# Kernel tuning notes

Measured on AMD Instinct MI355X. Metric: run time of the kernel, lower is better.

The kernel has to match this reference:

```python
import jax, jax.numpy as jnp
import numpy as np

N, IC, IH, IW = 8, 128, 32, 32
OC, H, KH, KW = 32, 256, 2, 2


def setup_inputs() -> dict:
    key = jax.random.key(0)
    ks = jax.random.split(key, 7)
    s1 = 1.0 / np.sqrt(IC)
    s2 = 1.0 / np.sqrt(H)
    x = jax.random.normal(ks[0], (N, IC, IH, IW), dtype=jnp.float32)
    # per-output-channel MLP params, stacked along oC (torch Linear-style uniform init)
    W1 = jax.random.uniform(ks[1], (OC, IC, H), jnp.float32, -s1, s1)
    b1 = jax.random.uniform(ks[2], (OC, H), jnp.float32, -s1, s1)
    W2 = jax.random.uniform(ks[3], (OC, H, H), jnp.float32, -s2, s2)
    b2 = jax.random.uniform(ks[4], (OC, H), jnp.float32, -s2, s2)
    W3 = jax.random.uniform(ks[5], (OC, H, KH * KW), jnp.float32, -s2, s2)
    b3 = jax.random.uniform(ks[6], (OC, KH * KW), jnp.float32, -s2, s2)
    return {"x": x, "W1": W1, "b1": b1, "W2": W2, "b2": b2, "W3": W3, "b3": b3}


def reference(x, W1, b1, W2, b2, W3, b3):
    n, iC, iH, iW = x.shape
    oC = W1.shape[0]
    kH, kW = KH, KW
    # per-pixel features: [n, iH, iW, iC]
    pix = jnp.transpose(x, (0, 2, 3, 1))
    # batched 3-layer MLP over stacked oC channels (single grouped GEMM per layer)
    h1 = jax.nn.relu(jnp.einsum('nijc,ocd->onijd', pix, W1) + b1[:, None, None, None, :])
    h2 = jax.nn.relu(jnp.einsum('onijd,ode->onije', h1, W2) + b2[:, None, None, None, :])
    out = jnp.einsum('onije,oek->onijk', h2, W3) + b3[:, None, None, None, :]
    # [oC, n, iH, iW, kH, kW] -> [n, oC, iH, kH, iW, kW] -> [n, oC, oH, oW]
    out = out.reshape(oC, n, iH, iW, kH, kW)
    out = jnp.transpose(out, (1, 0, 2, 4, 3, 5)).reshape(n, oC, kH * iH, kW * iW)
    return out
```

## Files before the change

### kernel.cpp

```cpp
#include <hip/hip_runtime.h>
#include <hip/hip_bf16.h>


#define IC    128
#define IHW   1024
#define OCH   32
#define HDIM  256

typedef float  f32x4  __attribute__((ext_vector_type(4)));
typedef float  f32x2  __attribute__((ext_vector_type(2)));
typedef __bf16 bf16x8 __attribute__((ext_vector_type(8)));
typedef unsigned short us8 __attribute__((ext_vector_type(8)));
typedef unsigned int u32;

static __device__ __forceinline__ unsigned short f2bf(float f) {
  __hip_bfloat16 h = __float2bfloat16(f);
  return __builtin_bit_cast(unsigned short, h);
}

static __device__ __forceinline__ u32 cvtpk(float lo, float hi) {
  u32 r;
  asm("v_cvt_pk_bf16_f32 %0, %1, %2" : "=v"(r) : "v"(lo), "v"(hi));
  return r;
}

static __device__ __forceinline__ bf16x8 ld16(const unsigned short* p) {
  return __builtin_bit_cast(bf16x8, *reinterpret_cast<const uint4*>(p));
}

static __device__ __forceinline__ void gl_lds16(const unsigned short* g, char* l) {
  __builtin_amdgcn_global_load_lds(
      (const __attribute__((address_space(1))) u32*)g,
      (__attribute__((address_space(3))) u32*)l,
      16, 0, 0);
}

__global__ __launch_bounds__(256) void transpose_bf16_k(
    const float* __restrict__ src, unsigned short* __restrict__ dst,
    int NR, int NC, int nrt, int nct)
{
  __shared__ float tl[64 * 65];
  const int bid = blockIdx.x;
  const int ct = bid % nct;
  const int rt = (bid / nct) % nrt;
  const int b  = bid / (nct * nrt);
  const int t  = threadIdx.x;

  const float* sb = src + ((size_t)b * NR + (rt << 6)) * NC + (ct << 6);
  const int col = (t & 15) << 2;
  const int rq  = t >> 4;
#pragma unroll
  for (int rr = 0; rr < 4; ++rr) {
    int row = (rr << 4) + rq;
    f32x4 v = *reinterpret_cast<const f32x4*>(sb + row * NC + col);
#pragma unroll
    for (int i = 0; i < 4; ++i) tl[row * 65 + col + i] = v[i];
  }
  __syncthreads();

  unsigned short* db = dst + ((size_t)b * NC + (ct << 6)) * NR + (rt << 6);
  const int r0 = (t & 7) << 3;
  const int cq = t >> 3;
#pragma unroll
  for (int cr = 0; cr < 2; ++cr) {
    int c = (cr << 5) + cq;
    us8 vv;
#pragma unroll
    for (int i = 0; i < 8; ++i) vv[i] = f2bf(tl[(r0 + i) * 65 + c]);
    *reinterpret_cast<us8*>(db + (size_t)c * NR + r0) = vv;
  }
}

__global__ void conv_w3_k(const float* __restrict__ W3, unsigned short* __restrict__ W3t) {
  int idx = blockIdx.x * 256 + threadIdx.x;
  int k = idx & 255;
  int nn = (idx >> 8) & 15;
  int o = idx >> 12;
  W3t[idx] = (nn < 4) ? f2bf(W3[(o * HDIM + k) * 4 + nn]) : (unsigned short)0;
}


#define LDB(dst, buf, ROW, ks)                                                   \
  _Pragma("unroll")                                                              \
  for (int mf = 0; mf < 2; ++mf) {                                               \
    int m = (mf << 4) + l15;                                                     \
    dst[mf] = *reinterpret_cast<const bf16x8*>(                                  \
        (buf) + ((((m << (ROW)) + ((ks) << 6) + (kgrp << 1))) ^ ((l15 & 7) << 4)));\
  }

#define MF4(WR, KS, BP)                                                          \
  __builtin_amdgcn_s_setprio(1);                                                 \
  _Pragma("unroll")                                                              \
  for (int nf = 0; nf < 2; ++nf)                                                 \
    _Pragma("unroll")                                                            \
    for (int mf = 0; mf < 2; ++mf)                                               \
      acc[nf][mf] = __builtin_amdgcn_mfma_f32_16x16x32_bf16(WR[nf][KS], BP[mf], acc[nf][mf], 0, 0, 0); \
  __builtin_amdgcn_s_setprio(0);

#define EPI(dst)                                                                 \
  _Pragma("unroll")                                                              \
  for (int nf = 0; nf < 2; ++nf) {                                               \
    int n0 = wnb + (nf << 4) + (lg << 2);                                        \
    _Pragma("unroll")                                                            \
    for (int mf = 0; mf < 2; ++mf) {                                             \
      int m = (mf << 4) + l15;                                                   \
      uint2 hv;                                                                  \
      hv.x = cvtpk(fmaxf(acc[nf][mf][0], 0.f), fmaxf(acc[nf][mf][1], 0.f));      \
      hv.y = cvtpk(fmaxf(acc[nf][mf][2], 0.f), fmaxf(acc[nf][mf][3], 0.f));      \
      *reinterpret_cast<uint2*>(                                                 \
          (dst) + (((m << 9) + (n0 << 1)) ^ ((l15 & 7) << 4))) = hv;             \
    }                                                                            \
  }

#define INIT_ACC(BB)                                                             \
  _Pragma("unroll")                                                              \
  for (int nf = 0; nf < 2; ++nf)                                                 \
    _Pragma("unroll")                                                            \
    for (int mf = 0; mf < 2; ++mf) acc[nf][mf] = BB[nf];

#define STAGE(PXB, BUF)                                                          \
  {                                                                              \
    int m = t >> 4, c16 = t & 15;                                                \
    gl_lds16(pix + (size_t)((PXB) + m) * IC + ((c16 ^ (m & 7)) << 3),            \
             (BUF) + t * 16);                                                    \
  }

__global__ __launch_bounds__(512, 2) void fused_mlp_k(
    const unsigned short* __restrict__ pix,
    const unsigned short* __restrict__ W1t,
    const unsigned short* __restrict__ W2t,
    const unsigned short* __restrict__ W3t,
    const float* __restrict__ b1,
    const float* __restrict__ b2,
    const float* __restrict__ b3f,
    float* __restrict__ out)
{
  __shared__ __align__(16) char lds[81920];
  const int t    = threadIdx.x;
  const int lane = t & 63;
  const int w    = t >> 6;
  const int bx   = blockIdx.x;
  const int o    = ((bx & 7) << 2) | ((bx >> 3) & 3);
  const int pixbase = (bx >> 5) << 8;

  const int l15  = lane & 15;
  const int lg   = lane >> 4;
  const int kgrp = lg << 3;
  const int wnb  = w << 5;

  char* pixb[2] = { lds,         lds + 8192 };
  char* h1b[2]  = { lds + 16384, lds + 32768 };
  char* h2b[2]  = { lds + 49152, lds + 65536 };

  STAGE(pixbase,      pixb[0])
  STAGE(pixbase + 32, pixb[1])

  const unsigned short* W1p = W1t + (o << 15) + (wnb + l15) * IC + kgrp;
  const unsigned short* W2p = W2t + (o << 16) + (wnb + l15) * HDIM + kgrp;
  bf16x8 W1r[2][4], W2r[2][8];
#pragma unroll
  for (int nf = 0; nf < 2; ++nf)
#pragma unroll
    for (int ks = 0; ks < 4; ++ks)
      W1r[nf][ks] = ld16(W1p + (nf << 4) * IC + (ks << 5));
#pragma unroll
  for (int nf = 0; nf < 2; ++nf)
#pragma unroll
    for (int ks = 0; ks < 8; ++ks)
      W2r[nf][ks] = ld16(W2p + (nf << 4) * HDIM + (ks << 5));

  f32x4 bb1[2], bb2[2];
#pragma unroll
  for (int nf = 0; nf < 2; ++nf) {
    bb1[nf] = *reinterpret_cast<const f32x4*>(b1 + (o << 8) + wnb + (nf << 4) + (lg << 2));
    bb2[nf] = *reinterpret_cast<const f32x4*>(b2 + (o << 8) + wnb + (nf << 4) + (lg << 2));
  }
  const f32x4 b3v = *reinterpret_cast<const f32x4*>(b3f + (o << 2));

  f32x4 acc[2][2];
  bf16x8 bp[2], bq[2];

  __syncthreads();

  INIT_ACC(bb1)
  LDB(bp, pixb[0], 8, 0)
  LDB(bq, pixb[0], 8, 1) MF4(W1r, 0, bp)
  LDB(bp, pixb[0], 8, 2) MF4(W1r, 1, bq)
  LDB(bq, pixb[0], 8, 3) MF4(W1r, 2, bp)
                         MF4(W1r, 3, bq)
  EPI(h1b[0])
  __syncthreads();

#pragma unroll
  for (int i = 0; i <= 8; ++i) {
    if (i <= 5) STAGE(pixbase + ((i + 2) << 5), pixb[i & 1])

    if (i <= 7) {
      char* src = h1b[i & 1];
      INIT_ACC(bb2)
      LDB(bp, src, 9, 0)
      LDB(bq, src, 9, 1) MF4(W2r, 0, bp)
      LDB(bp, src, 9, 2) MF4(W2r, 1, bq)
      LDB(bq, src, 9, 3) MF4(W2r, 2, bp)
      LDB(bp, src, 9, 4) MF4(W2r, 3, bq)
      LDB(bq, src, 9, 5) MF4(W2r, 4, bp)
      LDB(bp, src, 9, 6) MF4(W2r, 5, bq)
      LDB(bq, src, 9, 7) MF4(W2r, 6, bp)
                         MF4(W2r, 7, bq)
      EPI(h2b[i & 1])
    }

    if (i >= 1 && w < 2) {
      const char* hs = h2b[(i - 1) & 1];
      const unsigned short* W3p = W3t + (o << 12) + l15 * HDIM + kgrp;
      const int m3 = (w << 4) + l15;
      f32x4 a3a = b3v;
      f32x4 a3b = {0.f, 0.f, 0.f, 0.f};
      bf16x8 w3f0 = ld16(W3p), w3f1 = ld16(W3p + 32);
      bf16x8 bh0 = *reinterpret_cast<const bf16x8*>(
          hs + (((m3 << 9) + (kgrp << 1)) ^ ((l15 & 7) << 4)));
      bf16x8 bh1 = *reinterpret_cast<const bf16x8*>(
          hs + (((m3 << 9) + (1 << 6) + (kgrp << 1)) ^ ((l15 & 7) << 4)));
#pragma unroll
      for (int ks = 0; ks < 8; ks += 2) {
        bf16x8 wnA, bnA, wnB, bnB;
        if (ks < 6) {
          wnA = ld16(W3p + ((ks + 2) << 5));
          bnA = *reinterpret_cast<const bf16x8*>(
              hs + (((m3 << 9) + ((ks + 2) << 6) + (kgrp << 1)) ^ ((l15 & 7) << 4)));
          wnB = ld16(W3p + ((ks + 3) << 5));
          bnB = *reinterpret_cast<const bf16x8*>(
              hs + (((m3 << 9) + ((ks + 3) << 6) + (kgrp << 1)) ^ ((l15 & 7) << 4)));
        }
        a3a = __builtin_amdgcn_mfma_f32_16x16x32_bf16(w3f0, bh0, a3a, 0, 0, 0);
        a3b = __builtin_amdgcn_mfma_f32_16x16x32_bf16(w3f1, bh1, a3b, 0, 0, 0);
        w3f0 = wnA; bh0 = bnA; w3f1 = wnB; bh1 = bnB;
      }
      if (lane < 16) {
        int pixel = pixbase + ((i - 1) << 5) + m3;
        int n = pixel >> 10, p = pixel & 1023;
        int ii = p >> 5, jj = p & 31;
        float* ob = out + ((size_t)((n << 5) + o) << 12) + (ii << 7) + (jj << 1);
        f32x2 r0 = { a3a[0] + a3b[0], a3a[1] + a3b[1] };
        f32x2 r1 = { a3a[2] + a3b[2], a3a[3] + a3b[3] };
        *reinterpret_cast<f32x2*>(ob) = r0;
        *reinterpret_cast<f32x2*>(ob + 64) = r1;
      }
    }

    if (i <= 6) {
      char* psrc = pixb[(i + 1) & 1];
      INIT_ACC(bb1)
      LDB(bp, psrc, 8, 0)
      LDB(bq, psrc, 8, 1) MF4(W1r, 0, bp)
      LDB(bp, psrc, 8, 2) MF4(W1r, 1, bq)
      LDB(bq, psrc, 8, 3) MF4(W1r, 2, bp)
                          MF4(W1r, 3, bq)
      EPI(h1b[(i + 1) & 1])
    }

    __syncthreads();
  }
}

extern "C" void kernel_launch(void* const* d_in, const int* in_sizes, int n_in,
                              void* d_out, int out_size, void* d_ws, size_t ws_size,
                              hipStream_t stream) {
  const float* x  = (const float*)d_in[0];
  const float* W1 = (const float*)d_in[1];
  const float* b1 = (const float*)d_in[2];
  const float* W2 = (const float*)d_in[3];
  const float* b2 = (const float*)d_in[4];
  const float* W3 = (const float*)d_in[5];
  const float* b3 = (const float*)d_in[6];
  float* out = (float*)d_out;

  char* ws = (char*)d_ws;
  unsigned short* pixw = (unsigned short*)(ws);
  unsigned short* W1t  = (unsigned short*)(ws + (size_t)(2u << 20));
  unsigned short* W2t  = (unsigned short*)(ws + (size_t)(4u << 20));
  unsigned short* W3t  = (unsigned short*)(ws + (size_t)(8u << 20));

  transpose_bf16_k<<<8 * 2 * 16, 256, 0, stream>>>(x, pixw, 128, 1024, 2, 16);
  transpose_bf16_k<<<32 * 2 * 4, 256, 0, stream>>>(W1, W1t, 128, 256, 2, 4);
  transpose_bf16_k<<<32 * 4 * 4, 256, 0, stream>>>(W2, W2t, 256, 256, 4, 4);
  conv_w3_k<<<512, 256, 0, stream>>>(W3, W3t);

  fused_mlp_k<<<1024, 512, 0, stream>>>(pixw, W1t, W2t, W3t, b1, b2, b3, out);
}
```

Measured before the change: 92.79 us.

## Fuse layer-3 into layer-2 epilogue via register shuffles and partial sums

Instead of writing h2 to LDS and having two waves run the full K=256 layer-3 GEMM, each wave now converts its h2 accumulator slice to bf16 in registers. It rearranges that slice with cross-lane shuffles into an MFMA B-fragment and runs a single 16x16x32 MFMA against its slice of W3, which is held in a register. The per-wave partial outputs go to a small LDS buffer, and one wave sums the eight partials and adds the bias before storing. This removes the h2 LDS round trip, cuts LDS use from 80KB to 56KB, and spreads layer-3 work across all waves, at the cost of shuffle overhead and a serialized reduction done by a single wave.

```diff
diff --git a/kernel.cpp b/kernel.cpp
--- a/kernel.cpp
+++ b/kernel.cpp
@@ -135,7 +135,7 @@
     const float* __restrict__ b3f,
     float* __restrict__ out)
 {
-  __shared__ __align__(16) char lds[81920];
+  __shared__ __align__(16) char lds[57344];
   const int t    = threadIdx.x;
   const int lane = t & 63;
   const int w    = t >> 6;
@@ -150,7 +150,7 @@
 
   char* pixb[2] = { lds,         lds + 8192 };
   char* h1b[2]  = { lds + 16384, lds + 32768 };
-  char* h2b[2]  = { lds + 49152, lds + 65536 };
+  char* partb[2]= { lds + 49152, lds + 53248 };
 
   STAGE(pixbase,      pixb[0])
   STAGE(pixbase + 32, pixb[1])
@@ -169,6 +169,8 @@
     for (int ks = 0; ks < 8; ++ks)
       W2r[nf][ks] = ld16(W2p + (nf << 4) * HDIM + (ks << 5));
 
+  bf16x8 W3A = ld16(W3t + (o << 12) + l15 * HDIM + (w << 5) + kgrp);
+
   f32x4 bb1[2], bb2[2];
 #pragma unroll
   for (int nf = 0; nf < 2; ++nf) {
@@ -176,9 +178,14 @@
     bb2[nf] = *reinterpret_cast<const f32x4*>(b2 + (o << 8) + wnb + (nf << 4) + (lg << 2));
   }
   const f32x4 b3v = *reinterpret_cast<const f32x4*>(b3f + (o << 2));
+  const f32x4 vzero = {0.f, 0.f, 0.f, 0.f};
 
   f32x4 acc[2][2];
   bf16x8 bp[2], bq[2];
+
+  const int srcLo = (((lg << 1) & 3) << 4) + l15;
+  const int srcHi = ((((lg << 1) + 1) & 3) << 4) + l15;
+  const int sel   = lg >> 1;
 
   __syncthreads();
 
@@ -207,45 +214,46 @@
       LDB(bp, src, 9, 6) MF4(W2r, 5, bq)
       LDB(bq, src, 9, 7) MF4(W2r, 6, bp)
                          MF4(W2r, 7, bq)
-      EPI(h2b[i & 1])
+
+      char* pw = partb[i & 1];
+#pragma unroll
+      for (int mf = 0; mf < 2; ++mf) {
+        u32 p00 = cvtpk(fmaxf(acc[0][mf][0], 0.f), fmaxf(acc[0][mf][1], 0.f));
+        u32 p01 = cvtpk(fmaxf(acc[0][mf][2], 0.f), fmaxf(acc[0][mf][3], 0.f));
+        u32 p10 = cvtpk(fmaxf(acc[1][mf][0], 0.f), fmaxf(acc[1][mf][1], 0.f));
+        u32 p11 = cvtpk(fmaxf(acc[1][mf][2], 0.f), fmaxf(acc[1][mf][3], 0.f));
+        u32 a0 = __shfl((int)p00, srcLo, 64), c0 = __shfl((int)p10, srcLo, 64);
+        u32 a1 = __shfl((int)p01, srcLo, 64), c1 = __shfl((int)p11, srcLo, 64);
+        u32 a2 = __shfl((int)p00, srcHi, 64), c2 = __shfl((int)p10, srcHi, 64);
+        u32 a3 = __shfl((int)p01, srcHi, 64), c3 = __shfl((int)p11, srcHi, 64);
+        uint4 fr;
+        fr.x = sel ? c0 : a0;
+        fr.y = sel ? c1 : a1;
+        fr.z = sel ? c2 : a2;
+        fr.w = sel ? c3 : a3;
+        bf16x8 h2f = __builtin_bit_cast(bf16x8, fr);
+        f32x4 p3 = __builtin_amdgcn_mfma_f32_16x16x32_bf16(W3A, h2f, vzero, 0, 0, 0);
+        if (lane < 16)
+          *reinterpret_cast<f32x4*>(pw + (w << 9) + (mf << 8) + (l15 << 4)) = p3;
+      }
     }
 
-    if (i >= 1 && w < 2) {
-      const char* hs = h2b[(i - 1) & 1];
-      const unsigned short* W3p = W3t + (o << 12) + l15 * HDIM + kgrp;
-      const int m3 = (w << 4) + l15;
-      f32x4 a3a = b3v;
-      f32x4 a3b = {0.f, 0.f, 0.f, 0.f};
-      bf16x8 w3f0 = ld16(W3p), w3f1 = ld16(W3p + 32);
-      bf16x8 bh0 = *reinterpret_cast<const bf16x8*>(
-          hs + (((m3 << 9) + (kgrp << 1)) ^ ((l15 & 7) << 4)));
-      bf16x8 bh1 = *reinterpret_cast<const bf16x8*>(
-          hs + (((m3 << 9) + (1 << 6) + (kgrp << 1)) ^ ((l15 & 7) << 4)));
-#pragma unroll
-      for (int ks = 0; ks < 8; ks += 2) {
-        bf16x8 wnA, bnA, wnB, bnB;
-        if (ks < 6) {
-          wnA = ld16(W3p + ((ks + 2) << 5));
-          bnA = *reinterpret_cast<const bf16x8*>(
-              hs + (((m3 << 9) + ((ks + 2) << 6) + (kgrp << 1)) ^ ((l15 & 7) << 4)));
-          wnB = ld16(W3p + ((ks + 3) << 5));
-          bnB = *reinterpret_cast<const bf16x8*>(
-              hs + (((m3 << 9) + ((ks + 3) << 6) + (kgrp << 1)) ^ ((l15 & 7) << 4)));
-        }
-        a3a = __builtin_amdgcn_mfma_f32_16x16x32_bf16(w3f0, bh0, a3a, 0, 0, 0);
-        a3b = __builtin_amdgcn_mfma_f32_16x16x32_bf16(w3f1, bh1, a3b, 0, 0, 0);
-        w3f0 = wnA; bh0 = bnA; w3f1 = wnB; bh1 = bnB;
-      }
-      if (lane < 16) {
-        int pixel = pixbase + ((i - 1) << 5) + m3;
-        int n = pixel >> 10, p = pixel & 1023;
-        int ii = p >> 5, jj = p & 31;
-        float* ob = out + ((size_t)((n << 5) + o) << 12) + (ii << 7) + (jj << 1);
-        f32x2 r0 = { a3a[0] + a3b[0], a3a[1] + a3b[1] };
-        f32x2 r1 = { a3a[2] + a3b[2], a3a[3] + a3b[3] };
-        *reinterpret_cast<f32x2*>(ob) = r0;
-        *reinterpret_cast<f32x2*>(ob + 64) = r1;
-      }
+    if (i >= 1 && w == 7 && lane < 32) {
+      const char* pp = partb[(i - 1) & 1];
+      int px  = lane;
+      int mfp = px >> 4, l15p = px & 15;
+      f32x4 s = b3v;
+#pragma unroll
+      for (int ww = 0; ww < 8; ++ww)
+        s += *reinterpret_cast<const f32x4*>(pp + (ww << 9) + (mfp << 8) + (l15p << 4));
+      int pixel = pixbase + ((i - 1) << 5) + px;
+      int n = pixel >> 10, p = pixel & 1023;
+      int ii = p >> 5, jj = p & 31;
+      float* ob = out + ((size_t)((n << 5) + o) << 12) + (ii << 7) + (jj << 1);
+      f32x2 r0 = { s[0], s[1] };
+      f32x2 r1 = { s[2], s[3] };
+      *reinterpret_cast<f32x2*>(ob) = r0;
+      *reinterpret_cast<f32x2*>(ob + 64) = r1;
     }
 
     if (i <= 6) {
```

New measurement: 99.23 us. +6.9%, slower.

## Merge prepass kernels, triple-buffer pixel staging with vmcnt barriers, preload W3

Applied to the files above, without the earlier changes.

The four preprocessing launches (x, W1, W2 transposes and W3 conversion) become one prepass kernel that branches on block index, which cuts launch overhead. The fused MLP kernel now triple-buffers the pixel tiles in LDS and issues each prefetch later in the iteration. Its __syncthreads is replaced by a barrier that waits only on outstanding global loads up to a count, so one prefetch can stay in flight across the barrier. W3 fragments are loaded into registers once instead of on every iteration, which raises register pressure and LDS use (90 KB) at two blocks per CU.

```diff
diff --git a/kernel.cpp b/kernel.cpp
--- a/kernel.cpp
+++ b/kernel.cpp
@@ -35,48 +35,60 @@
       16, 0, 0);
 }
 
-__global__ __launch_bounds__(256) void transpose_bf16_k(
-    const float* __restrict__ src, unsigned short* __restrict__ dst,
-    int NR, int NC, int nrt, int nct)
+static __device__ void transpose_dev(const float* __restrict__ src,
+                                     unsigned short* __restrict__ dst,
+                                     int NR, int NC, int nrt, int nct,
+                                     int bid, int t, float* tl)
+{
+  const int ct = bid % nct;
+  const int rt = (bid / nct) % nrt;
+  const int b  = bid / (nct * nrt);
+
+  const float* sb = src + ((size_t)b * NR + (rt << 6)) * NC + (ct << 6);
+  const int col = (t & 15) << 2;
+  const int rq  = t >> 4;
+#pragma unroll
+  for (int rr = 0; rr < 4; ++rr) {
+    int row = (rr << 4) + rq;
+    f32x4 v = *reinterpret_cast<const f32x4*>(sb + row * NC + col);
+#pragma unroll
+    for (int i = 0; i < 4; ++i) tl[row * 65 + col + i] = v[i];
+  }
+  __syncthreads();
+
+  unsigned short* db = dst + ((size_t)b * NC + (ct << 6)) * NR + (rt << 6);
+  const int r0 = (t & 7) << 3;
+  const int cq = t >> 3;
+#pragma unroll
+  for (int cr = 0; cr < 2; ++cr) {
+    int c = (cr << 5) + cq;
+    us8 vv;
+#pragma unroll
+    for (int i = 0; i < 8; ++i) vv[i] = f2bf(tl[(r0 + i) * 65 + c]);
+    *reinterpret_cast<us8*>(db + (size_t)c * NR + r0) = vv;
+  }
+}
+
+__global__ __launch_bounds__(256) void prepass_k(
+    const float* __restrict__ x,  unsigned short* __restrict__ pix,
+    const float* __restrict__ W1, unsigned short* __restrict__ W1t,
+    const float* __restrict__ W2, unsigned short* __restrict__ W2t,
+    const float* __restrict__ W3, unsigned short* __restrict__ W3t)
 {
   __shared__ float tl[64 * 65];
   const int bid = blockIdx.x;
-  const int ct = bid % nct;
-  const int rt = (bid / nct) % nrt;
-  const int b  = bid / (nct * nrt);
-  const int t  = threadIdx.x;
-
-  const float* sb = src + ((size_t)b * NR + (rt << 6)) * NC + (ct << 6);
-  const int col = (t & 15) << 2;
-  const int rq  = t >> 4;
-#pragma unroll
-  for (int rr = 0; rr < 4; ++rr) {
-    int row = (rr << 4) + rq;
-    f32x4 v = *reinterpret_cast<const f32x4*>(sb + row * NC + col);
-#pragma unroll
-    for (int i = 0; i < 4; ++i) tl[row * 65 + col + i] = v[i];
-  }
-  __syncthreads();
-
-  unsigned short* db = dst + ((size_t)b * NC + (ct << 6)) * NR + (rt << 6);
-  const int r0 = (t & 7) << 3;
-  const int cq = t >> 3;
-#pragma unroll
-  for (int cr = 0; cr < 2; ++cr) {
-    int c = (cr << 5) + cq;
-    us8 vv;
-#pragma unroll
-    for (int i = 0; i < 8; ++i) vv[i] = f2bf(tl[(r0 + i) * 65 + c]);
-    *reinterpret_cast<us8*>(db + (size_t)c * NR + r0) = vv;
-  }
-}
-
-__global__ void conv_w3_k(const float* __restrict__ W3, unsigned short* __restrict__ W3t) {
-  int idx = blockIdx.x * 256 + threadIdx.x;
-  int k = idx & 255;
-  int nn = (idx >> 8) & 15;
-  int o = idx >> 12;
-  W3t[idx] = (nn < 4) ? f2bf(W3[(o * HDIM + k) * 4 + nn]) : (unsigned short)0;
+  const int t   = threadIdx.x;
+  if (bid < 256) {
+    transpose_dev(x, pix, 128, 1024, 2, 16, bid, t, tl);
+  } else if (bid < 512) {
+    transpose_dev(W1, W1t, 128, 256, 2, 4, bid - 256, t, tl);
+  } else if (bid < 1024) {
+    transpose_dev(W2, W2t, 256, 256, 4, 4, bid - 512, t, tl);
+  } else {
+    int idx = ((bid - 1024) << 8) + t;
+    int k = idx & 255, nn = (idx >> 8) & 15, o = idx >> 12;
+    W3t[idx] = (nn < 4) ? f2bf(W3[(o * HDIM + k) * 4 + nn]) : (unsigned short)0;
+  }
 }
 
 
@@ -125,6 +137,12 @@
              (BUF) + t * 16);                                                    \
   }
 
+#define PIPE_BARRIER(N)                                                          \
+  asm volatile("s_waitcnt vmcnt(" #N ") lgkmcnt(0)" ::: "memory");               \
+  __builtin_amdgcn_sched_barrier(0);                                             \
+  __builtin_amdgcn_s_barrier();                                                  \
+  __builtin_amdgcn_sched_barrier(0);
+
 __global__ __launch_bounds__(512, 2) void fused_mlp_k(
     const unsigned short* __restrict__ pix,
     const unsigned short* __restrict__ W1t,
@@ -135,7 +153,7 @@
     const float* __restrict__ b3f,
     float* __restrict__ out)
 {
-  __shared__ __align__(16) char lds[81920];
+  __shared__ __align__(16) char lds[90112];
   const int t    = threadIdx.x;
   const int lane = t & 63;
   const int w    = t >> 6;
@@ -148,16 +166,17 @@
   const int kgrp = lg << 3;
   const int wnb  = w << 5;
 
-  char* pixb[2] = { lds,         lds + 8192 };
-  char* h1b[2]  = { lds + 16384, lds + 32768 };
-  char* h2b[2]  = { lds + 49152, lds + 65536 };
+  char* pixb[3] = { lds, lds + 8192, lds + 16384 };
+  char* h1b[2]  = { lds + 24576, lds + 40960 };
+  char* h2b[2]  = { lds + 57344, lds + 73728 };
 
   STAGE(pixbase,      pixb[0])
   STAGE(pixbase + 32, pixb[1])
+  STAGE(pixbase + 64, pixb[2])
 
   const unsigned short* W1p = W1t + (o << 15) + (wnb + l15) * IC + kgrp;
   const unsigned short* W2p = W2t + (o << 16) + (wnb + l15) * HDIM + kgrp;
-  bf16x8 W1r[2][4], W2r[2][8];
+  bf16x8 W1r[2][4], W2r[2][8], W3r[8];
 #pragma unroll
   for (int nf = 0; nf < 2; ++nf)
 #pragma unroll
@@ -168,6 +187,9 @@
 #pragma unroll
     for (int ks = 0; ks < 8; ++ks)
       W2r[nf][ks] = ld16(W2p + (nf << 4) * HDIM + (ks << 5));
+#pragma unroll
+  for (int ks = 0; ks < 8; ++ks)
+    W3r[ks] = ld16(W3t + (o << 12) + l15 * HDIM + (ks << 5) + kgrp);
 
   f32x4 bb1[2], bb2[2];
 #pragma unroll
@@ -176,6 +198,7 @@
     bb2[nf] = *reinterpret_cast<const f32x4*>(b2 + (o << 8) + wnb + (nf << 4) + (lg << 2));
   }
   const f32x4 b3v = *reinterpret_cast<const f32x4*>(b3f + (o << 2));
+  const f32x4 vzero = {0.f, 0.f, 0.f, 0.f};
 
   f32x4 acc[2][2];
   bf16x8 bp[2], bq[2];
@@ -193,8 +216,6 @@
 
 #pragma unroll
   for (int i = 0; i <= 8; ++i) {
-    if (i <= 5) STAGE(pixbase + ((i + 2) << 5), pixb[i & 1])
-
     if (i <= 7) {
       char* src = h1b[i & 1];
       INIT_ACC(bb2)
@@ -212,29 +233,17 @@
 
     if (i >= 1 && w < 2) {
       const char* hs = h2b[(i - 1) & 1];
-      const unsigned short* W3p = W3t + (o << 12) + l15 * HDIM + kgrp;
       const int m3 = (w << 4) + l15;
       f32x4 a3a = b3v;
       f32x4 a3b = {0.f, 0.f, 0.f, 0.f};
-      bf16x8 w3f0 = ld16(W3p), w3f1 = ld16(W3p + 32);
-      bf16x8 bh0 = *reinterpret_cast<const bf16x8*>(
-          hs + (((m3 << 9) + (kgrp << 1)) ^ ((l15 & 7) << 4)));
-      bf16x8 bh1 = *reinterpret_cast<const bf16x8*>(
-          hs + (((m3 << 9) + (1 << 6) + (kgrp << 1)) ^ ((l15 & 7) << 4)));
 #pragma unroll
       for (int ks = 0; ks < 8; ks += 2) {
-        bf16x8 wnA, bnA, wnB, bnB;
-        if (ks < 6) {
-          wnA = ld16(W3p + ((ks + 2) << 5));
-          bnA = *reinterpret_cast<const bf16x8*>(
-              hs + (((m3 << 9) + ((ks + 2) << 6) + (kgrp << 1)) ^ ((l15 & 7) << 4)));
-          wnB = ld16(W3p + ((ks + 3) << 5));
-          bnB = *reinterpret_cast<const bf16x8*>(
-              hs + (((m3 << 9) + ((ks + 3) << 6) + (kgrp << 1)) ^ ((l15 & 7) << 4)));
-        }
-        a3a = __builtin_amdgcn_mfma_f32_16x16x32_bf16(w3f0, bh0, a3a, 0, 0, 0);
-        a3b = __builtin_amdgcn_mfma_f32_16x16x32_bf16(w3f1, bh1, a3b, 0, 0, 0);
-        w3f0 = wnA; bh0 = bnA; w3f1 = wnB; bh1 = bnB;
+        bf16x8 bh0 = *reinterpret_cast<const bf16x8*>(
+            hs + (((m3 << 9) + (ks << 6) + (kgrp << 1)) ^ ((l15 & 7) << 4)));
+        bf16x8 bh1 = *reinterpret_cast<const bf16x8*>(
+            hs + (((m3 << 9) + ((ks + 1) << 6) + (kgrp << 1)) ^ ((l15 & 7) << 4)));
+        a3a = __builtin_amdgcn_mfma_f32_16x16x32_bf16(W3r[ks],     bh0, a3a, 0, 0, 0);
+        a3b = __builtin_amdgcn_mfma_f32_16x16x32_bf16(W3r[ks + 1], bh1, a3b, 0, 0, 0);
       }
       if (lane < 16) {
         int pixel = pixbase + ((i - 1) << 5) + m3;
@@ -248,8 +257,10 @@
       }
     }
 
+    if (i <= 4) STAGE(pixbase + ((i + 3) << 5), pixb[i % 3])
+
     if (i <= 6) {
-      char* psrc = pixb[(i + 1) & 1];
+      char* psrc = pixb[(i + 1) % 3];
       INIT_ACC(bb1)
       LDB(bp, psrc, 8, 0)
       LDB(bq, psrc, 8, 1) MF4(W1r, 0, bp)
@@ -259,7 +270,7 @@
       EPI(h1b[(i + 1) & 1])
     }
 
-    __syncthreads();
+    if (i <= 4) { PIPE_BARRIER(1) } else { PIPE_BARRIER(0) }
   }
 }
 
@@ -281,10 +292,6 @@
   unsigned short* W2t  = (unsigned short*)(ws + (size_t)(4u << 20));
   unsigned short* W3t  = (unsigned short*)(ws + (size_t)(8u << 20));
 
-  transpose_bf16_k<<<8 * 2 * 16, 256, 0, stream>>>(x, pixw, 128, 1024, 2, 16);
-  transpose_bf16_k<<<32 * 2 * 4, 256, 0, stream>>>(W1, W1t, 128, 256, 2, 4);
-  transpose_bf16_k<<<32 * 4 * 4, 256, 0, stream>>>(W2, W2t, 256, 256, 4, 4);
-  conv_w3_k<<<512, 256, 0, stream>>>(W3, W3t);
-
+  prepass_k<<<1536, 256, 0, stream>>>(x, pixw, W1, W1t, W2, W2t, W3, W3t);
   fused_mlp_k<<<1024, 512, 0, stream>>>(pixw, W1t, W2t, W3t, b1, b2, b3, out);
 }
```

New measurement: 86.13 us. 7.2% less time.
